# Performance work log

Measured on AMD Instinct MI355X. Metric: run time of the kernel, lower is better.

Reference implementation:

```python
import jax, jax.numpy as jnp
import numpy as np

KERNEL_SIZE = 37  # int((6*20-7)//3) = 37, already odd
PAD = (KERNEL_SIZE - 1) // 2  # 18


def moving_avg(x):
    """Edge-replicated moving average along token axis. x: [B, T, C]."""
    front = jnp.repeat(x[:, :1, :], PAD, axis=1)
    end = jnp.repeat(x[:, -1:, :], PAD, axis=1)
    xp = jnp.concatenate([front, x, end], axis=1)  # [B, T+2*PAD, C]
    cs = jnp.cumsum(xp, axis=1)
    cs = jnp.concatenate([jnp.zeros_like(cs[:, :1, :]), cs], axis=1)
    # window sums: length (T+2*PAD+1) - KERNEL_SIZE = T
    return (cs[:, KERNEL_SIZE:, :] - cs[:, :-KERNEL_SIZE, :]) / KERNEL_SIZE


def setup_inputs() -> dict:
    key = jax.random.key(0)
    ks = jax.random.split(key, 5)
    B, T, Cin, Cout = 4096, 17, 512, 512
    scale = 1.0 / np.sqrt(Cin)
    x = jax.random.normal(ks[0], (B, T, Cin), dtype=jnp.float32)
    W_seasonal = jax.random.uniform(ks[1], (T, Cout, Cin), jnp.float32, -scale, scale)
    b_seasonal = jax.random.uniform(ks[2], (T, Cout), jnp.float32, -scale, scale)
    W_trend = jax.random.uniform(ks[3], (T, Cout, Cin), jnp.float32, -scale, scale)
    b_trend = jax.random.uniform(ks[4], (T, Cout), jnp.float32, -scale, scale)
    return {"x": x, "W_seasonal": W_seasonal, "b_seasonal": b_seasonal,
            "W_trend": W_trend, "b_trend": b_trend}


def reference(x, W_seasonal, b_seasonal, W_trend, b_trend):
    trend = moving_avg(x)            # [B, T, Cin]
    seasonal = x - trend             # [B, T, Cin]
    # per-token (grouped) linear layers as one batched einsum
    s_out = jnp.einsum('btc,tdc->btd', seasonal, W_seasonal) + b_seasonal[None]
    t_out = jnp.einsum('btc,tdc->btd', trend, W_trend) + b_trend[None]
    return s_out + t_out
```

## Files before the change

### kernel.cpp

```cpp
#include <hip/hip_runtime.h>
#include <stdint.h>

#define B_N 4096
#define T_N 17
#define C_N 512
#define KTOT 1024

typedef __bf16 bf16x8 __attribute__((ext_vector_type(8)));
typedef float  f32x4  __attribute__((ext_vector_type(4)));

__device__ __forceinline__ unsigned short f2b(float f){
  unsigned u = __float_as_uint(f);
  return (unsigned short)((u + 0x7fffu + ((u >> 16) & 1u)) >> 16);
}
__device__ __forceinline__ unsigned pk2(float a, float b){
  return (unsigned)f2b(a) | ((unsigned)f2b(b) << 16);
}

__device__ __forceinline__ void gll16(const void* g, void* l){
  __builtin_amdgcn_global_load_lds(
      (const __attribute__((address_space(1))) unsigned int*)g,
      (__attribute__((address_space(3))) unsigned int*)l, 16, 0, 0);
}

#define BAR()   __builtin_amdgcn_s_barrier()
#define LGKM0() do{ asm volatile("s_waitcnt lgkmcnt(0)" ::: "memory"); \
                    __builtin_amdgcn_sched_barrier(0); }while(0)
#define VMC(n)  do{ asm volatile("s_waitcnt vmcnt(" #n ")" ::: "memory"); \
                    __builtin_amdgcn_sched_barrier(0); }while(0)

__global__ __launch_bounds__(256) void prep_w(
    const float* __restrict__ Ws, const float* __restrict__ Wt,
    unsigned short* __restrict__ wcat)
{
  const size_t i8 = ((size_t)blockIdx.x * 256 + threadIdx.x) * 8;
  const int t   = (int)(i8 >> 18);
  const int rem = (int)(i8 & 262143);
  const int d   = rem >> 9;
  const int c   = rem & 511;
  float4 a0 = *(const float4*)(Ws + i8);
  float4 a1 = *(const float4*)(Ws + i8 + 4);
  float4 b0 = *(const float4*)(Wt + i8);
  float4 b1 = *(const float4*)(Wt + i8 + 4);
  uint4 oa, od;
  oa.x = pk2(a0.x, a0.y); oa.y = pk2(a0.z, a0.w);
  oa.z = pk2(a1.x, a1.y); oa.w = pk2(a1.z, a1.w);
  od.x = pk2(b0.x - a0.x, b0.y - a0.y); od.y = pk2(b0.z - a0.z, b0.w - a0.w);
  od.z = pk2(b1.x - a1.x, b1.y - a1.y); od.w = pk2(b1.z - a1.z, b1.w - a1.w);
  unsigned short* base = wcat + ((size_t)(t * C_N + d)) * KTOT + c;
  *(uint4*)base = oa;
  *(uint4*)(base + C_N) = od;
}

__global__ __launch_bounds__(256) void prep_bsum(
    const float* __restrict__ bs, const float* __restrict__ bt, float* __restrict__ o)
{
  const int i = blockIdx.x * 256 + threadIdx.x;
  o[i] = bs[i] + bt[i];
}

__global__ __launch_bounds__(256) void prep_a(
    const float* __restrict__ x, unsigned short* __restrict__ acat)
{
  const int idx = blockIdx.x * 256 + threadIdx.x;
  const int b = idx >> 6;
  const int c = (idx & 63) << 3;
  const float* xp = x + (size_t)b * (T_N * C_N) + c;
  float s[8] = {0,0,0,0,0,0,0,0};
  float f0[8], fl[8];
#pragma unroll
  for (int tt = 0; tt < T_N; ++tt){
    float4 w0 = *(const float4*)(xp + (size_t)tt * C_N);
    float4 w1 = *(const float4*)(xp + (size_t)tt * C_N + 4);
    float f[8] = {w0.x, w0.y, w0.z, w0.w, w1.x, w1.y, w1.z, w1.w};
    uint4 o;
    o.x = pk2(f[0],f[1]); o.y = pk2(f[2],f[3]);
    o.z = pk2(f[4],f[5]); o.w = pk2(f[6],f[7]);
    *(uint4*)(acat + ((size_t)tt * B_N + b) * KTOT + c) = o;
    if (tt == 0){
#pragma unroll
      for (int i=0;i<8;++i) f0[i] = f[i];
    }
    if (tt == T_N-1){
#pragma unroll
      for (int i=0;i<8;++i) fl[i] = f[i];
    }
#pragma unroll
    for (int i=0;i<8;++i) s[i] += f[i];
  }
  const float inv = 1.0f / 37.0f;
  float uu[8], vv[8];
#pragma unroll
  for (int i=0;i<8;++i){
    uu[i] = (s[i] + 18.0f * f0[i] + 2.0f * fl[i]) * inv;
    vv[i] = (fl[i] - f0[i]) * inv;
  }
#pragma unroll
  for (int tt = 0; tt < T_N; ++tt){
    const float tfv = (float)tt;
    float tr[8];
#pragma unroll
    for (int i=0;i<8;++i) tr[i] = fmaf(tfv, vv[i], uu[i]);
    uint4 o;
    o.x = pk2(tr[0],tr[1]); o.y = pk2(tr[2],tr[3]);
    o.z = pk2(tr[4],tr[5]); o.w = pk2(tr[6],tr[7]);
    *(uint4*)(acat + ((size_t)tt * B_N + b) * KTOT + C_N + c) = o;
  }
}

__global__ __launch_bounds__(512) void gemm8(
    const unsigned short* __restrict__ acat,
    const unsigned short* __restrict__ wcat,
    const float* __restrict__ bsum,
    float* __restrict__ out)
{
  __shared__ alignas(16) unsigned short A_lds[2][256][64];
  __shared__ alignas(16) unsigned short B_lds[2][256][64];

  const int tid = threadIdx.x;
  const int bid = blockIdx.x;
  const int wg = (bid & 7) * 68 + (bid >> 3);
  const int t  = wg >> 5;
  const int mt = (wg >> 1) & 15;
  const int nt = wg & 1;
  const int m0 = mt << 8;
  const int n0 = nt << 8;

  const int lane = tid & 63;
  const int wave = tid >> 6;
  const int wr = wave >> 2;
  const int wc = wave & 3;
  const int lr = lane & 15;
  const int g  = lane >> 4;

  const int row0 = tid >> 3;
  const int cc0  = tid & 7;
  const int cswz = ((cc0 ^ (row0 & 7)) << 3);
  const unsigned short* gA0 = acat + ((size_t)t * B_N + m0 + row0) * KTOT + cswz;
  const unsigned short* gB0 = wcat + ((size_t)t * C_N + n0 + row0) * KTOT + cswz;
  unsigned short* lA0 = &A_lds[0][row0][cc0 << 3];
  unsigned short* lB0 = &B_lds[0][row0][cc0 << 3];

  auto stageA = [&](int bb, int kt){
#pragma unroll
    for (int r = 0; r < 4; ++r)
      gll16(gA0 + (size_t)kt * 64 + r * 65536, lA0 + bb * 16384 + r * 4096);
  };
  auto stageB = [&](int bb, int kt){
#pragma unroll
    for (int r = 0; r < 4; ++r)
      gll16(gB0 + (size_t)kt * 64 + r * 65536, lB0 + bb * 16384 + r * 4096);
  };

  const int sw  = lr & 7;
  const int ca0 = (( g     ) ^ sw) << 3;
  const int ca1 = ((4 | g  ) ^ sw) << 3;
  const unsigned short* Arow = &A_lds[0][wr * 128 + lr][0];
  const unsigned short* Brow = &B_lds[0][wc * 64  + lr][0];

  f32x4 acc[8][4];
#pragma unroll
  for (int i=0;i<8;++i)
#pragma unroll
    for (int j=0;j<4;++j){ f32x4 z = {0.f,0.f,0.f,0.f}; acc[i][j] = z; }

  auto rdA4 = [&](bf16x8 (&dst)[4][2], int bb, int mih){
    const unsigned short* p = Arow + bb * 16384 + mih * 1024;
#pragma unroll
    for (int mi=0;mi<4;++mi){
      dst[mi][0] = *(const bf16x8*)(p + mi * 1024 + ca0);
      dst[mi][1] = *(const bf16x8*)(p + mi * 1024 + ca1);
    }
  };
  auto rdB2 = [&](bf16x8 (&dst)[2][2], int bb, int nih){
    const unsigned short* p = Brow + bb * 16384 + nih * 1024;
#pragma unroll
    for (int ni=0;ni<2;++ni){
      dst[ni][0] = *(const bf16x8*)(p + ni * 1024 + ca0);
      dst[ni][1] = *(const bf16x8*)(p + ni * 1024 + ca1);
    }
  };

  auto group = [&](int bb, int kn, bool st, bool last){
    bf16x8 aL[4][2], aH[4][2], b01[2][2], b23[2][2];
    rdA4(aL, bb, 0); rdB2(b01, bb, 0);
    BAR(); LGKM0();
    __builtin_amdgcn_s_setprio(1);
#pragma unroll
    for (int mi=0;mi<4;++mi)
#pragma unroll
      for (int ni=0;ni<2;++ni){
        acc[mi][ni] = __builtin_amdgcn_mfma_f32_16x16x32_bf16(aL[mi][0], b01[ni][0], acc[mi][ni],0,0,0);
        acc[mi][ni] = __builtin_amdgcn_mfma_f32_16x16x32_bf16(aL[mi][1], b01[ni][1], acc[mi][ni],0,0,0);
      }
    __builtin_amdgcn_s_setprio(0);
    BAR();
    rdB2(b23, bb, 2);
    BAR(); LGKM0();
    __builtin_amdgcn_s_setprio(1);
#pragma unroll
    for (int mi=0;mi<4;++mi)
#pragma unroll
      for (int ni=0;ni<2;++ni){
        acc[mi][2+ni] = __builtin_amdgcn_mfma_f32_16x16x32_bf16(aL[mi][0], b23[ni][0], acc[mi][2+ni],0,0,0);
        acc[mi][2+ni] = __builtin_amdgcn_mfma_f32_16x16x32_bf16(aL[mi][1], b23[ni][1], acc[mi][2+ni],0,0,0);
      }
    __builtin_amdgcn_s_setprio(0);
    BAR();
    if (st) stageB(bb, kn);
    rdA4(aH, bb, 4);
    BAR(); LGKM0();
    __builtin_amdgcn_s_setprio(1);
#pragma unroll
    for (int mi=0;mi<4;++mi)
#pragma unroll
      for (int ni=0;ni<2;++ni){
        acc[4+mi][ni] = __builtin_amdgcn_mfma_f32_16x16x32_bf16(aH[mi][0], b01[ni][0], acc[4+mi][ni],0,0,0);
        acc[4+mi][ni] = __builtin_amdgcn_mfma_f32_16x16x32_bf16(aH[mi][1], b01[ni][1], acc[4+mi][ni],0,0,0);
      }
    __builtin_amdgcn_s_setprio(0);
    BAR();
    if (st) stageA(bb, kn);
    BAR();
    __builtin_amdgcn_s_setprio(1);
#pragma unroll
    for (int mi=0;mi<4;++mi)
#pragma unroll
      for (int ni=0;ni<2;++ni){
        acc[4+mi][2+ni] = __builtin_amdgcn_mfma_f32_16x16x32_bf16(aH[mi][0], b23[ni][0], acc[4+mi][2+ni],0,0,0);
        acc[4+mi][2+ni] = __builtin_amdgcn_mfma_f32_16x16x32_bf16(aH[mi][1], b23[ni][1], acc[4+mi][2+ni],0,0,0);
      }
    __builtin_amdgcn_s_setprio(0);
    if (last) { VMC(0); } else { VMC(8); }
    BAR();
  };

  stageB(0, 0); stageA(0, 0);
  stageB(1, 1); stageA(1, 1);
  VMC(8);
  BAR();

#pragma unroll 1
  for (int it = 0; it < 8; ++it){
    const bool st   = it < 7;
    const bool last = it == 7;
    group(0, 2*it + 2, st, last);
    group(1, 2*it + 3, st, last);
  }

  float bias[4];
#pragma unroll
  for (int ni=0;ni<4;++ni)
    bias[ni] = bsum[(size_t)t * C_N + n0 + wc*64 + ni*16 + lr];

#pragma unroll
  for (int mi=0;mi<8;++mi){
#pragma unroll
    for (int rr=0;rr<4;++rr){
      const int m = m0 + wr*128 + mi*16 + g*4 + rr;
      float* op = out + ((size_t)m * T_N + t) * C_N + n0 + wc*64 + lr;
#pragma unroll
      for (int ni=0;ni<4;++ni)
        op[ni*16] = acc[mi][ni][rr] + bias[ni];
    }
  }
}

extern "C" void kernel_launch(void* const* d_in, const int* in_sizes, int n_in,
                              void* d_out, int out_size, void* d_ws, size_t ws_size,
                              hipStream_t stream)
{
  const float* x   = (const float*)d_in[0];
  const float* Wsl = (const float*)d_in[1];
  const float* bsl = (const float*)d_in[2];
  const float* Wtr = (const float*)d_in[3];
  const float* btr = (const float*)d_in[4];
  float* out = (float*)d_out;

  const size_t WCAT_BYTES = (size_t)T_N * C_N * KTOT * 2;
  const size_t BS_BYTES   = (size_t)T_N * C_N * 4;
  char* ws = (char*)d_ws;
  unsigned short* wcat = (unsigned short*)ws;
  float*          bsum = (float*)(ws + WCAT_BYTES);
  unsigned short* acat = (unsigned short*)(ws + WCAT_BYTES + BS_BYTES);

  prep_w  <<<dim3(2176), dim3(256), 0, stream>>>(Wsl, Wtr, wcat);
  prep_bsum<<<dim3(34),  dim3(256), 0, stream>>>(bsl, btr, bsum);
  prep_a  <<<dim3(1024), dim3(256), 0, stream>>>(x, acat);
  gemm8   <<<dim3(544),  dim3(512), 0, stream>>>(acat, wcat, bsum, out);
  (void)in_sizes; (void)n_in; (void)out_size; (void)ws_size;
}
```

Baseline: 409.6 us.

## Restructure GEMM main loop into single-phase compute with fewer barriers

Replaces the four-phase interleaved group (LDS reads, barriers and staging between MFMA quarters) with one loop iteration per K-block. All B fragments and the low A fragments are read up front, the high A read sits mid-loop, and staging of the next buffers happens after one barrier at the end. This cuts barriers per K-step and lets the compiler schedule LDS reads around the MFMAs. It adds launch_bounds(512,2) to push for two blocks per CU. The trade-off is less overlap between global staging and compute, plus register pressure under the occupancy hint, which could spill.

```diff
diff --git a/kernel.cpp b/kernel.cpp
--- a/kernel.cpp
+++ b/kernel.cpp
@@ -24,10 +24,9 @@
 }
 
 #define BAR()   __builtin_amdgcn_s_barrier()
-#define LGKM0() do{ asm volatile("s_waitcnt lgkmcnt(0)" ::: "memory"); \
-                    __builtin_amdgcn_sched_barrier(0); }while(0)
 #define VMC(n)  do{ asm volatile("s_waitcnt vmcnt(" #n ")" ::: "memory"); \
                     __builtin_amdgcn_sched_barrier(0); }while(0)
+#define FENCE() asm volatile("" ::: "memory")
 
 __global__ __launch_bounds__(256) void prep_w(
     const float* __restrict__ Ws, const float* __restrict__ Wt,
@@ -108,7 +107,7 @@
   }
 }
 
-__global__ __launch_bounds__(512) void gemm8(
+__global__ __launch_bounds__(512, 2) void gemm8(
     const unsigned short* __restrict__ acat,
     const unsigned short* __restrict__ wcat,
     const float* __restrict__ bsum,
@@ -181,71 +180,54 @@
     }
   };
 
-  auto group = [&](int bb, int kn, bool st, bool last){
-    bf16x8 aL[4][2], aH[4][2], b01[2][2], b23[2][2];
-    rdA4(aL, bb, 0); rdB2(b01, bb, 0);
-    BAR(); LGKM0();
-    __builtin_amdgcn_s_setprio(1);
-#pragma unroll
-    for (int mi=0;mi<4;++mi)
-#pragma unroll
-      for (int ni=0;ni<2;++ni){
-        acc[mi][ni] = __builtin_amdgcn_mfma_f32_16x16x32_bf16(aL[mi][0], b01[ni][0], acc[mi][ni],0,0,0);
-        acc[mi][ni] = __builtin_amdgcn_mfma_f32_16x16x32_bf16(aL[mi][1], b01[ni][1], acc[mi][ni],0,0,0);
-      }
-    __builtin_amdgcn_s_setprio(0);
-    BAR();
-    rdB2(b23, bb, 2);
-    BAR(); LGKM0();
-    __builtin_amdgcn_s_setprio(1);
-#pragma unroll
-    for (int mi=0;mi<4;++mi)
-#pragma unroll
-      for (int ni=0;ni<2;++ni){
-        acc[mi][2+ni] = __builtin_amdgcn_mfma_f32_16x16x32_bf16(aL[mi][0], b23[ni][0], acc[mi][2+ni],0,0,0);
-        acc[mi][2+ni] = __builtin_amdgcn_mfma_f32_16x16x32_bf16(aL[mi][1], b23[ni][1], acc[mi][2+ni],0,0,0);
-      }
-    __builtin_amdgcn_s_setprio(0);
-    BAR();
-    if (st) stageB(bb, kn);
-    rdA4(aH, bb, 4);
-    BAR(); LGKM0();
-    __builtin_amdgcn_s_setprio(1);
-#pragma unroll
-    for (int mi=0;mi<4;++mi)
-#pragma unroll
-      for (int ni=0;ni<2;++ni){
-        acc[4+mi][ni] = __builtin_amdgcn_mfma_f32_16x16x32_bf16(aH[mi][0], b01[ni][0], acc[4+mi][ni],0,0,0);
-        acc[4+mi][ni] = __builtin_amdgcn_mfma_f32_16x16x32_bf16(aH[mi][1], b01[ni][1], acc[4+mi][ni],0,0,0);
-      }
-    __builtin_amdgcn_s_setprio(0);
-    BAR();
-    if (st) stageA(bb, kn);
-    BAR();
-    __builtin_amdgcn_s_setprio(1);
-#pragma unroll
-    for (int mi=0;mi<4;++mi)
-#pragma unroll
-      for (int ni=0;ni<2;++ni){
-        acc[4+mi][2+ni] = __builtin_amdgcn_mfma_f32_16x16x32_bf16(aH[mi][0], b23[ni][0], acc[4+mi][2+ni],0,0,0);
-        acc[4+mi][2+ni] = __builtin_amdgcn_mfma_f32_16x16x32_bf16(aH[mi][1], b23[ni][1], acc[4+mi][2+ni],0,0,0);
-      }
-    __builtin_amdgcn_s_setprio(0);
-    if (last) { VMC(0); } else { VMC(8); }
-    BAR();
-  };
-
   stageB(0, 0); stageA(0, 0);
   stageB(1, 1); stageA(1, 1);
   VMC(8);
   BAR();
 
 #pragma unroll 1
-  for (int it = 0; it < 8; ++it){
-    const bool st   = it < 7;
-    const bool last = it == 7;
-    group(0, 2*it + 2, st, last);
-    group(1, 2*it + 3, st, last);
+  for (int it = 0; it < 16; ++it){
+    const int bb = it & 1;
+    bf16x8 b01[2][2], b23[2][2], aL[4][2], aH[4][2];
+
+    rdB2(b01, bb, 0);
+    rdB2(b23, bb, 2);
+    rdA4(aL, bb, 0);
+
+    __builtin_amdgcn_s_setprio(1);
+#pragma unroll
+    for (int mi=0;mi<4;++mi){
+      if (mi == 2) rdA4(aH, bb, 4);
+#pragma unroll
+      for (int ni=0;ni<2;++ni){
+        acc[mi][ni]   = __builtin_amdgcn_mfma_f32_16x16x32_bf16(aL[mi][0], b01[ni][0], acc[mi][ni],0,0,0);
+        acc[mi][ni]   = __builtin_amdgcn_mfma_f32_16x16x32_bf16(aL[mi][1], b01[ni][1], acc[mi][ni],0,0,0);
+        acc[mi][2+ni] = __builtin_amdgcn_mfma_f32_16x16x32_bf16(aL[mi][0], b23[ni][0], acc[mi][2+ni],0,0,0);
+        acc[mi][2+ni] = __builtin_amdgcn_mfma_f32_16x16x32_bf16(aL[mi][1], b23[ni][1], acc[mi][2+ni],0,0,0);
+      }
+    }
+#pragma unroll
+    for (int mi=0;mi<4;++mi){
+#pragma unroll
+      for (int ni=0;ni<2;++ni){
+        acc[4+mi][ni]   = __builtin_amdgcn_mfma_f32_16x16x32_bf16(aH[mi][0], b01[ni][0], acc[4+mi][ni],0,0,0);
+        acc[4+mi][ni]   = __builtin_amdgcn_mfma_f32_16x16x32_bf16(aH[mi][1], b01[ni][1], acc[4+mi][ni],0,0,0);
+        acc[4+mi][2+ni] = __builtin_amdgcn_mfma_f32_16x16x32_bf16(aH[mi][0], b23[ni][0], acc[4+mi][2+ni],0,0,0);
+        acc[4+mi][2+ni] = __builtin_amdgcn_mfma_f32_16x16x32_bf16(aH[mi][1], b23[ni][1], acc[4+mi][2+ni],0,0,0);
+      }
+    }
+    __builtin_amdgcn_s_setprio(0);
+
+    FENCE();
+    BAR();
+    if (it < 14){
+      stageB(bb, it + 2);
+      stageA(bb, it + 2);
+      VMC(8);
+    } else if (it == 14){
+      VMC(0);
+    }
+    BAR();
   }
 
   float bias[4];
```

Result: slower. 423.9 us (+3.5%).
